# Optimization experiments

Measured on AMD Instinct MI355X. Metric: run time of the kernel, lower is better.

Reference implementation:

```python
import jax, jax.numpy as jnp
import numpy as np

N = 50000      # nodes
E = 800000     # edges (avg degree 16)
D = 128        # embed_dim
H = 8          # nhead
HD = D // H    # head dim = 16


def setup_inputs() -> dict:
    key = jax.random.key(0)
    ks = jax.random.split(key, 6)
    s = 1.0 / np.sqrt(D)  # ~xavier scale for square matrices
    return {
        "feats": jax.random.normal(ks[0], (N, D), jnp.float32),
        "edge_index": jax.random.randint(ks[1], (E, 2), 0, N, dtype=jnp.int64),
        "Wq": jax.random.normal(ks[2], (D, D), jnp.float32) * s,
        "bq": jnp.zeros((D,), jnp.float32),
        "Wk": jax.random.normal(ks[3], (D, D), jnp.float32) * s,
        "bk": jnp.zeros((D,), jnp.float32),
        "Wv": jax.random.normal(ks[4], (D, D), jnp.float32) * s,
        "bv": jnp.zeros((D,), jnp.float32),
        "Wo": jax.random.normal(ks[5], (D, D), jnp.float32) * s,
        "bo": jnp.zeros((D,), jnp.float32),
    }


def reference(feats, edge_index, Wq, bq, Wk, bk, Wv, bv, Wo, bo):
    # Projections (nn.Linear: x @ W.T + b), split into heads: [N, H, HD]
    q = (feats @ Wq.T + bq).reshape(N, H, HD)
    k = (feats @ Wk.T + bk).reshape(N, H, HD)
    v = (feats @ Wv.T + bv).reshape(N, H, HD)

    r = edge_index[:, 0]  # source nodes
    c = edge_index[:, 1]  # destination nodes (softmax / aggregation groups)

    # Per-edge, per-head dot-product scores: [E, H]
    scores = jnp.einsum('ehd,ehd->eh', q[c], k[r]) / np.sqrt(HD)

    # Custom scatter-softmax: src_max clamped to min 0; extra exp(-src_max) in denom
    smax = jnp.maximum(jax.ops.segment_max(scores, c, num_segments=N), 0.0)  # [N, H]
    ex = jnp.exp(scores - smax[c])                                           # [E, H]
    denom = jax.ops.segment_sum(ex, c, num_segments=N)                       # [N, H]
    attn = ex / (denom + jnp.exp(-smax))[c]                                  # [E, H]

    # Weighted V per edge, scatter-mean to destination nodes
    out_e = attn[:, :, None] * v[r]                      # [E, H, HD]
    agg = jax.ops.segment_sum(out_e, c, num_segments=N)  # [N, H, HD]
    cnt = jax.ops.segment_sum(jnp.ones((E,), jnp.float32), c, num_segments=N)
    agg = agg / jnp.maximum(cnt, 1.0)[:, None, None]

    return agg.reshape(N, D) @ Wo.T + bo
```

## Files before the change

kernel.cpp:

```cpp
#include <hip/hip_runtime.h>
#include <hip/hip_bf16.h>

#define N_NODES 50000
#define N_EDGES 800000
#define DIM 128
#define NHEAD 8
#define HDIM 16
#define ELL_PAD 64
#define ELL_SLICES 391
#define ELL_BLOCKS (8 * ELL_SLICES)
#define ROWTILES 3125
#define QKV_TPB 8
#define QKV_GROUPS ((ROWTILES + QKV_TPB - 1) / QKV_TPB)
#define QKV_GRID (QKV_GROUPS * 3)
#define OUT_BLOCKS ((ROWTILES + 3) / 4)

#define Q_OFF      0ull
#define KV_OFF     12800000ull
#define AGG_OFF    38400000ull
#define ELL_OFF    51200000ull
#define CNT_OFF    64000000ull
#define WBF_OFF    64200192ull
#define BIAS_OFF   64331264ull


typedef __attribute__((ext_vector_type(8))) short short8;
typedef __attribute__((ext_vector_type(4))) float floatx4;

__device__ inline float bflo2f(unsigned u) { return __uint_as_float(u << 16); }
__device__ inline float bfhi2f(unsigned u) { return __uint_as_float(u & 0xffff0000u); }
__device__ inline unsigned short f2bf(float f) {
    unsigned u = __float_as_uint(f);
    return (unsigned short)((u + 0x7fffu + ((u >> 16) & 1u)) >> 16);
}

__device__ inline void detect_flags(const void* feats, const void* edge,
                                    int& isbf, int& is32) {
    const unsigned short* f = (const unsigned short*)feats;
    const unsigned int* eg = (const unsigned int*)edge;
    int lane = threadIdx.x & 63;
    unsigned e = (f[lane] >> 7) & 0xFF;
    int junk = (e >= 0x90 || (e > 0 && e <= 0x60)) ? 1 : 0;
    unsigned long long jm = __ballot(junk);
    int nz = (lane < 32 && eg[2 * lane + 1] != 0) ? 1 : 0;
    unsigned long long nm = __ballot(nz);
    isbf = (jm == 0ull) ? 1 : 0;
    is32 = (nm != 0ull) ? 1 : 0;
}

__device__ inline void load_edge(const int* edge, int is32, int e, int& r, int& c) {
    if (is32) { int2 p = ((const int2*)edge)[e]; r = p.x; c = p.y; }
    else {
        const long long* p = (const long long*)edge;
        r = (int)p[2 * e]; c = (int)p[2 * e + 1];
    }
    if ((unsigned)r >= N_NODES) r = 0;
    if ((unsigned)c >= N_NODES) c = 0;
}

__device__ inline float ldf(const void* p, int isbf, int i) {
    return isbf ? __bfloat162float(((const __hip_bfloat16*)p)[i])
                : ((const float*)p)[i];
}

__device__ inline short8 ldfrag(const void* base, int isbf, size_t off) {
    if (isbf) return *(const short8*)((const unsigned short*)base + off);
    const float* f = (const float*)base + off;
    float4 f0 = *(const float4*)f;
    float4 f1 = *(const float4*)(f + 4);
    short8 a;
    a[0] = (short)f2bf(f0.x); a[1] = (short)f2bf(f0.y);
    a[2] = (short)f2bf(f0.z); a[3] = (short)f2bf(f0.w);
    a[4] = (short)f2bf(f1.x); a[5] = (short)f2bf(f1.y);
    a[6] = (short)f2bf(f1.z); a[7] = (short)f2bf(f1.w);
    return a;
}

__global__ __launch_bounds__(256) void ell_build(const void* feats, const int* edge,
                                                 const void* wq, const void* wk,
                                                 const void* wv, const void* wo,
                                                 const void* bq, const void* bk,
                                                 const void* bv, const void* bo,
                                                 int* cnt, int* ell,
                                                 unsigned short* wbf, float* bias) {
    int isbf, is32; detect_flags(feats, edge, isbf, is32);

    if (blockIdx.x >= ELL_BLOCKS) {
        int b2 = blockIdx.x - ELL_BLOCKS;
        if (b2 == 256) {
            for (int j = threadIdx.x; j < 512; j += 256) {
                int m2 = j >> 7;
                const void* bb = (m2 == 0) ? bq : (m2 == 1) ? bk : (m2 == 2) ? bv : bo;
                bias[j] = ldf(bb, isbf, j & 127);
            }
            return;
        }
        if (isbf) return;
        int idx = b2 * 256 + (int)threadIdx.x;
        int mm = idx >> 14, rem = idx & 16383;
        const void* wsrc = (mm == 0) ? wq : (mm == 1) ? wk : (mm == 2) ? wv : wo;
        wbf[idx] = f2bf(((const float*)wsrc)[rem]);
        return;
    }

    int pid = blockIdx.x & 7, slice = blockIdx.x >> 3;
    int base = slice * 2048 + (int)threadIdx.x;
    #pragma unroll
    for (int j = 0; j < 8; ++j) {
        int e = base + j * 256;
        if (e < N_EDGES) {
            int r, c; load_edge(edge, is32, e, r, c);
            if ((c & 7) == pid) {
                int slot = atomicAdd(cnt + c, 1);
                if (slot < ELL_PAD) ell[c * ELL_PAD + slot] = r;
            }
        }
    }
}

__global__ __launch_bounds__(256) void qkv_mfma(const void* feats_raw, const int* edge,
                                                const void* wq_raw, const void* wk_raw,
                                                const void* wv_raw,
                                                const unsigned short* wbf,
                                                const float* bias,
                                                unsigned short* q_s, unsigned short* kv_s) {
    int isbf, is32; detect_flags(feats_raw, edge, isbf, is32);
    int grp = blockIdx.x % QKV_GROUPS;
    int m   = blockIdx.x / QKV_GROUPS;
    int wv  = threadIdx.x >> 6;
    int lane = threadIdx.x & 63;
    int mrow = lane & 15, quad = lane >> 4;

    int rt0 = grp * QKV_TPB + wv * 2;
    int rt1 = rt0 + 1;
    bool v0 = rt0 < ROWTILES, v1 = rt1 < ROWTILES;

    short8 a0[4], a1[4];
    {
        size_t ar0 = (size_t)(v0 ? rt0 : 0) * 16 + mrow;
        size_t ar1 = (size_t)(v1 ? rt1 : 0) * 16 + mrow;
        #pragma unroll
        for (int kt = 0; kt < 4; ++kt) {
            a0[kt] = ldfrag(feats_raw, isbf, ar0 * DIM + quad * 8 + kt * 32);
            a1[kt] = ldfrag(feats_raw, isbf, ar1 * DIM + quad * 8 + kt * 32);
        }
    }

    const void* wraw = (m == 0) ? wq_raw : (m == 1) ? wk_raw : wv_raw;
    const unsigned short* wm = isbf ? (const unsigned short*)wraw : wbf + m * 16384;
    int pbase = (m == 2) ? 2 : 0;
    int piece = pbase + (mrow >> 3);
    int d = mrow & 7;

    for (int nt = 0; nt < 8; ++nt) {
        float b = bias[m * 128 + nt * 16 + mrow];
        floatx4 ac0 = {b, b, b, b};
        floatx4 ac1 = {b, b, b, b};
        const unsigned short* wp = wm + (size_t)(nt * 16 + mrow) * DIM + quad * 8;
        #pragma unroll
        for (int kt = 0; kt < 4; ++kt) {
            short8 bf = *(const short8*)(wp + kt * 32);
            ac0 = __builtin_amdgcn_mfma_f32_16x16x32_bf16(a0[kt], bf, ac0, 0, 0, 0);
            ac1 = __builtin_amdgcn_mfma_f32_16x16x32_bf16(a1[kt], bf, ac1, 0, 0, 0);
        }
        if (m == 0) {
            if (v0) {
                #pragma unroll
                for (int r4 = 0; r4 < 4; ++r4)
                    q_s[(size_t)(rt0 * 16 + quad * 4 + r4) * DIM + nt * 16 + mrow] = f2bf(ac0[r4]);
            }
            if (v1) {
                #pragma unroll
                for (int r4 = 0; r4 < 4; ++r4)
                    q_s[(size_t)(rt1 * 16 + quad * 4 + r4) * DIM + nt * 16 + mrow] = f2bf(ac1[r4]);
            }
        } else {
            if (v0) {
                #pragma unroll
                for (int r4 = 0; r4 < 4; ++r4)
                    kv_s[(size_t)(rt0 * 16 + quad * 4 + r4) * 256 + piece * 64 + nt * 8 + d] = f2bf(ac0[r4]);
            }
            if (v1) {
                #pragma unroll
                for (int r4 = 0; r4 < 4; ++r4)
                    kv_s[(size_t)(rt1 * 16 + quad * 4 + r4) * 256 + piece * 64 + nt * 8 + d] = f2bf(ac1[r4]);
            }
        }
    }
}

__global__ __launch_bounds__(256) void node_agg(const int* __restrict__ cnt,
                                                const int* __restrict__ ell,
                                                const unsigned short* __restrict__ q_s,
                                                const uint4* __restrict__ kvpack,
                                                uint4* __restrict__ agg_bf) {
    int node = (blockIdx.x * 256 + threadIdx.x) >> 6;
    int lane = threadIdx.x & 63;
    if (node >= N_NODES) return;
    int e = lane >> 3, h = lane & 7;

    const uint4* qp = (const uint4*)(q_s + (size_t)node * DIM + h * HDIM);
    uint4 q0 = qp[0], q1 = qp[1];
    float qv[16];
    qv[0]  = bflo2f(q0.x); qv[1]  = bfhi2f(q0.x);
    qv[2]  = bflo2f(q0.y); qv[3]  = bfhi2f(q0.y);
    qv[4]  = bflo2f(q0.z); qv[5]  = bfhi2f(q0.z);
    qv[6]  = bflo2f(q0.w); qv[7]  = bfhi2f(q0.w);
    qv[8]  = bflo2f(q1.x); qv[9]  = bfhi2f(q1.x);
    qv[10] = bflo2f(q1.y); qv[11] = bfhi2f(q1.y);
    qv[12] = bflo2f(q1.z); qv[13] = bfhi2f(q1.z);
    qv[14] = bflo2f(q1.w); qv[15] = bfhi2f(q1.w);

    int degt = cnt[node];
    int deg = degt < ELL_PAD ? degt : ELL_PAD;
    float l = 0.f;
    float acc[16];
    #pragma unroll
    for (int i = 0; i < 16; ++i) acc[i] = 0.f;

    const int* erow = ell + node * ELL_PAD;
    for (int i0 = 0; i0 < deg; i0 += 16) {
        int i1 = i0 + e, i2 = i0 + 8 + e;
        bool ok1 = i1 < deg, ok2 = i2 < deg;
        int r1 = ok1 ? erow[i1] : 0;
        int r2 = ok2 ? erow[i2] : 0;
        const uint4* kp1 = kvpack + (size_t)r1 * 32;
        const uint4* kp2 = kvpack + (size_t)r2 * 32;
        uint4 ka1 = kp1[h], kb1 = kp1[8 + h], va1 = kp1[16 + h], vb1 = kp1[24 + h];
        uint4 ka2 = kp2[h], kb2 = kp2[8 + h], va2 = kp2[16 + h], vb2 = kp2[24 + h];

        float s1 = 0.f;
        s1 += bflo2f(ka1.x) * qv[0]  + bfhi2f(ka1.x) * qv[1];
        s1 += bflo2f(ka1.y) * qv[2]  + bfhi2f(ka1.y) * qv[3];
        s1 += bflo2f(ka1.z) * qv[4]  + bfhi2f(ka1.z) * qv[5];
        s1 += bflo2f(ka1.w) * qv[6]  + bfhi2f(ka1.w) * qv[7];
        s1 += bflo2f(kb1.x) * qv[8]  + bfhi2f(kb1.x) * qv[9];
        s1 += bflo2f(kb1.y) * qv[10] + bfhi2f(kb1.y) * qv[11];
        s1 += bflo2f(kb1.z) * qv[12] + bfhi2f(kb1.z) * qv[13];
        s1 += bflo2f(kb1.w) * qv[14] + bfhi2f(kb1.w) * qv[15];
        float p1 = ok1 ? __expf(s1 * 0.25f) : 0.f;
        l += p1;
        acc[0]  += p1 * bflo2f(va1.x); acc[1]  += p1 * bfhi2f(va1.x);
        acc[2]  += p1 * bflo2f(va1.y); acc[3]  += p1 * bfhi2f(va1.y);
        acc[4]  += p1 * bflo2f(va1.z); acc[5]  += p1 * bfhi2f(va1.z);
        acc[6]  += p1 * bflo2f(va1.w); acc[7]  += p1 * bfhi2f(va1.w);
        acc[8]  += p1 * bflo2f(vb1.x); acc[9]  += p1 * bfhi2f(vb1.x);
        acc[10] += p1 * bflo2f(vb1.y); acc[11] += p1 * bfhi2f(vb1.y);
        acc[12] += p1 * bflo2f(vb1.z); acc[13] += p1 * bfhi2f(vb1.z);
        acc[14] += p1 * bflo2f(vb1.w); acc[15] += p1 * bfhi2f(vb1.w);

        float s2 = 0.f;
        s2 += bflo2f(ka2.x) * qv[0]  + bfhi2f(ka2.x) * qv[1];
        s2 += bflo2f(ka2.y) * qv[2]  + bfhi2f(ka2.y) * qv[3];
        s2 += bflo2f(ka2.z) * qv[4]  + bfhi2f(ka2.z) * qv[5];
        s2 += bflo2f(ka2.w) * qv[6]  + bfhi2f(ka2.w) * qv[7];
        s2 += bflo2f(kb2.x) * qv[8]  + bfhi2f(kb2.x) * qv[9];
        s2 += bflo2f(kb2.y) * qv[10] + bfhi2f(kb2.y) * qv[11];
        s2 += bflo2f(kb2.z) * qv[12] + bfhi2f(kb2.z) * qv[13];
        s2 += bflo2f(kb2.w) * qv[14] + bfhi2f(kb2.w) * qv[15];
        float p2 = ok2 ? __expf(s2 * 0.25f) : 0.f;
        l += p2;
        acc[0]  += p2 * bflo2f(va2.x); acc[1]  += p2 * bfhi2f(va2.x);
        acc[2]  += p2 * bflo2f(va2.y); acc[3]  += p2 * bfhi2f(va2.y);
        acc[4]  += p2 * bflo2f(va2.z); acc[5]  += p2 * bfhi2f(va2.z);
        acc[6]  += p2 * bflo2f(va2.w); acc[7]  += p2 * bfhi2f(va2.w);
        acc[8]  += p2 * bflo2f(vb2.x); acc[9]  += p2 * bfhi2f(vb2.x);
        acc[10] += p2 * bflo2f(vb2.y); acc[11] += p2 * bfhi2f(vb2.y);
        acc[12] += p2 * bflo2f(vb2.z); acc[13] += p2 * bfhi2f(vb2.z);
        acc[14] += p2 * bflo2f(vb2.w); acc[15] += p2 * bfhi2f(vb2.w);
    }

    #pragma unroll
    for (int m = 8; m < 64; m <<= 1) {
        l += __shfl_xor(l, m);
        #pragma unroll
        for (int i = 0; i < 16; ++i) acc[i] += __shfl_xor(acc[i], m);
    }

    float inv = 1.0f / ((1.0f + l) * (float)(degt > 0 ? degt : 1));
    if (e == 0) {
        unsigned o[8];
        #pragma unroll
        for (int i = 0; i < 8; ++i)
            o[i] = (unsigned)f2bf(acc[2 * i] * inv) | ((unsigned)f2bf(acc[2 * i + 1] * inv) << 16);
        uint4* op = agg_bf + (size_t)node * 16 + h * 2;
        op[0] = make_uint4(o[0], o[1], o[2], o[3]);
        op[1] = make_uint4(o[4], o[5], o[6], o[7]);
    }
}

__global__ __launch_bounds__(256) void out_mfma(const unsigned short* agg_bf,
                                                const void* feats, const int* edge,
                                                const void* wo_raw,
                                                const unsigned short* wbf,
                                                const float* bias, void* out) {
    int isbf, is32; detect_flags(feats, edge, isbf, is32);
    const unsigned short* W = isbf ? (const unsigned short*)wo_raw : wbf + 3 * 16384;
    int rowtile = blockIdx.x * 4 + (threadIdx.x >> 6);
    int lane = threadIdx.x & 63;
    int mrow = lane & 15, quad = lane >> 4;
    bool valid = rowtile < ROWTILES;
    size_t arow = (size_t)(valid ? rowtile : 0) * 16 + mrow;

    short8 a[4];
    const unsigned short* ap = agg_bf + arow * DIM + quad * 8;
    #pragma unroll
    for (int kt = 0; kt < 4; ++kt) a[kt] = *(const short8*)(ap + kt * 32);

    for (int nt = 0; nt < 8; nt += 2) {
        float b0 = bias[3 * 128 + nt * 16 + mrow];
        float b1 = bias[3 * 128 + (nt + 1) * 16 + mrow];
        floatx4 ac0 = {b0, b0, b0, b0};
        floatx4 ac1 = {b1, b1, b1, b1};
        const unsigned short* wp0 = W + (size_t)(nt * 16 + mrow) * DIM + quad * 8;
        const unsigned short* wp1 = W + (size_t)((nt + 1) * 16 + mrow) * DIM + quad * 8;
        #pragma unroll
        for (int kt = 0; kt < 4; ++kt) {
            short8 f0 = *(const short8*)(wp0 + kt * 32);
            short8 f1 = *(const short8*)(wp1 + kt * 32);
            ac0 = __builtin_amdgcn_mfma_f32_16x16x32_bf16(a[kt], f0, ac0, 0, 0, 0);
            ac1 = __builtin_amdgcn_mfma_f32_16x16x32_bf16(a[kt], f1, ac1, 0, 0, 0);
        }
        if (valid) {
            if (isbf) {
                #pragma unroll
                for (int r4 = 0; r4 < 4; ++r4) {
                    int row = rowtile * 16 + quad * 4 + r4;
                    ((unsigned short*)out)[(size_t)row * DIM + nt * 16 + mrow] = f2bf(ac0[r4]);
                    ((unsigned short*)out)[(size_t)row * DIM + (nt + 1) * 16 + mrow] = f2bf(ac1[r4]);
                }
            } else {
                #pragma unroll
                for (int r4 = 0; r4 < 4; ++r4) {
                    int row = rowtile * 16 + quad * 4 + r4;
                    ((float*)out)[(size_t)row * DIM + nt * 16 + mrow] = ac0[r4];
                    ((float*)out)[(size_t)row * DIM + (nt + 1) * 16 + mrow] = ac1[r4];
                }
            }
        }
    }
}

extern "C" void kernel_launch(void* const* d_in, const int* in_sizes, int n_in,
                              void* d_out, int out_size, void* d_ws, size_t ws_size,
                              hipStream_t stream) {
    const void* feats = d_in[0];
    const int*  edge  = (const int*)d_in[1];
    const void* Wq = d_in[2]; const void* bq = d_in[3];
    const void* Wk = d_in[4]; const void* bk = d_in[5];
    const void* Wv = d_in[6]; const void* bv = d_in[7];
    const void* Wo = d_in[8]; const void* bo = d_in[9];

    char* ws = (char*)d_ws;
    unsigned short* q_s  = (unsigned short*)(ws + Q_OFF);
    unsigned short* kv_s = (unsigned short*)(ws + KV_OFF);
    unsigned short* aggb = (unsigned short*)(ws + AGG_OFF);
    int* ell             = (int*)(ws + ELL_OFF);
    int* cnt             = (int*)(ws + CNT_OFF);
    unsigned short* wbf  = (unsigned short*)(ws + WBF_OFF);
    float* bias          = (float*)(ws + BIAS_OFF);

    hipMemsetAsync(ws + CNT_OFF, 0, N_NODES * 4, stream);

    ell_build<<<ELL_BLOCKS + 257, 256, 0, stream>>>(feats, edge, Wq, Wk, Wv, Wo,
                                                    bq, bk, bv, bo, cnt, ell,
                                                    wbf, bias);

    qkv_mfma<<<QKV_GRID, 256, 0, stream>>>(feats, edge, Wq, Wk, Wv, wbf, bias,
                                           q_s, kv_s);

    node_agg<<<(N_NODES * 64 + 255) / 256, 256, 0, stream>>>(cnt, ell, q_s,
                                                             (const uint4*)(ws + KV_OFF),
                                                             (uint4*)aggb);

    out_mfma<<<OUT_BLOCKS, 256, 0, stream>>>(aggb, feats, edge, Wo, wbf, bias, d_out);
}
```

Measured before the change: 241.4 us.

## Merge ELL build and QKV projection into one launch; pack bf16 math into float2

The ELL construction, weight conversion and QKV MFMA projection now run as separate block ranges of one kernel, so they overlap and one launch boundary disappears. The QKV blocks therefore convert raw weights and biases themselves through ldfrag/ldf instead of reading the pre-converted wbf buffer. The node aggregation loop is rewritten with float2 vectors, so the compiler can emit packed FMA instructions for the dot products and V accumulation. The cost is redundant fp32-to-bf16 weight conversion in every QKV block, and a different summation order in the scores.

```diff
diff --git a/kernel.cpp b/kernel.cpp
--- a/kernel.cpp
+++ b/kernel.cpp
@@ -13,6 +13,8 @@
 #define QKV_TPB 8
 #define QKV_GROUPS ((ROWTILES + QKV_TPB - 1) / QKV_TPB)
 #define QKV_GRID (QKV_GROUPS * 3)
+#define WBF_BLOCKS 257
+#define PREP_GRID (ELL_BLOCKS + WBF_BLOCKS + QKV_GRID)
 #define OUT_BLOCKS ((ROWTILES + 3) / 4)
 
 #define Q_OFF      0ull
@@ -26,12 +28,19 @@
 
 typedef __attribute__((ext_vector_type(8))) short short8;
 typedef __attribute__((ext_vector_type(4))) float floatx4;
+typedef __attribute__((ext_vector_type(2))) float floatx2;
 
 __device__ inline float bflo2f(unsigned u) { return __uint_as_float(u << 16); }
 __device__ inline float bfhi2f(unsigned u) { return __uint_as_float(u & 0xffff0000u); }
 __device__ inline unsigned short f2bf(float f) {
     unsigned u = __float_as_uint(f);
     return (unsigned short)((u + 0x7fffu + ((u >> 16) & 1u)) >> 16);
+}
+__device__ inline floatx2 bfpair(unsigned u) {
+    floatx2 r;
+    r.x = __uint_as_float(u << 16);
+    r.y = __uint_as_float(u & 0xffff0000u);
+    return r;
 }
 
 __device__ inline void detect_flags(const void* feats, const void* edge,
@@ -76,17 +85,36 @@
     return a;
 }
 
-__global__ __launch_bounds__(256) void ell_build(const void* feats, const int* edge,
-                                                 const void* wq, const void* wk,
-                                                 const void* wv, const void* wo,
-                                                 const void* bq, const void* bk,
-                                                 const void* bv, const void* bo,
-                                                 int* cnt, int* ell,
-                                                 unsigned short* wbf, float* bias) {
-    int isbf, is32; detect_flags(feats, edge, isbf, is32);
-
-    if (blockIdx.x >= ELL_BLOCKS) {
-        int b2 = blockIdx.x - ELL_BLOCKS;
+__global__ __launch_bounds__(256) void prep(const void* feats_raw, const int* edge,
+                                            const void* wq_raw, const void* wk_raw,
+                                            const void* wv_raw, const void* wo_raw,
+                                            const void* bq, const void* bk,
+                                            const void* bv, const void* bo,
+                                            int* cnt, int* ell,
+                                            unsigned short* wbf, float* bias,
+                                            unsigned short* q_s, unsigned short* kv_s) {
+    int isbf, is32; detect_flags(feats_raw, edge, isbf, is32);
+    int blk = blockIdx.x;
+
+    if (blk < ELL_BLOCKS) {
+        int pid = blk & 7, slice = blk >> 3;
+        int base = slice * 2048 + (int)threadIdx.x;
+        #pragma unroll
+        for (int j = 0; j < 8; ++j) {
+            int e = base + j * 256;
+            if (e < N_EDGES) {
+                int r, c; load_edge(edge, is32, e, r, c);
+                if ((c & 7) == pid) {
+                    int slot = atomicAdd(cnt + c, 1);
+                    if (slot < ELL_PAD) ell[c * ELL_PAD + slot] = r;
+                }
+            }
+        }
+        return;
+    }
+
+    if (blk < ELL_BLOCKS + WBF_BLOCKS) {
+        int b2 = blk - ELL_BLOCKS;
         if (b2 == 256) {
             for (int j = threadIdx.x; j < 512; j += 256) {
                 int m2 = j >> 7;
@@ -98,35 +126,14 @@
         if (isbf) return;
         int idx = b2 * 256 + (int)threadIdx.x;
         int mm = idx >> 14, rem = idx & 16383;
-        const void* wsrc = (mm == 0) ? wq : (mm == 1) ? wk : (mm == 2) ? wv : wo;
+        const void* wsrc = (mm == 0) ? wq_raw : (mm == 1) ? wk_raw : (mm == 2) ? wv_raw : wo_raw;
         wbf[idx] = f2bf(((const float*)wsrc)[rem]);
         return;
     }
 
-    int pid = blockIdx.x & 7, slice = blockIdx.x >> 3;
-    int base = slice * 2048 + (int)threadIdx.x;
-    #pragma unroll
-    for (int j = 0; j < 8; ++j) {
-        int e = base + j * 256;
-        if (e < N_EDGES) {
-            int r, c; load_edge(edge, is32, e, r, c);
-            if ((c & 7) == pid) {
-                int slot = atomicAdd(cnt + c, 1);
-                if (slot < ELL_PAD) ell[c * ELL_PAD + slot] = r;
-            }
-        }
-    }
-}
-
-__global__ __launch_bounds__(256) void qkv_mfma(const void* feats_raw, const int* edge,
-                                                const void* wq_raw, const void* wk_raw,
-                                                const void* wv_raw,
-                                                const unsigned short* wbf,
-                                                const float* bias,
-                                                unsigned short* q_s, unsigned short* kv_s) {
-    int isbf, is32; detect_flags(feats_raw, edge, isbf, is32);
-    int grp = blockIdx.x % QKV_GROUPS;
-    int m   = blockIdx.x / QKV_GROUPS;
+    int qb = blk - ELL_BLOCKS - WBF_BLOCKS;
+    int grp = qb % QKV_GROUPS;
+    int m   = qb / QKV_GROUPS;
     int wv  = threadIdx.x >> 6;
     int lane = threadIdx.x & 63;
     int mrow = lane & 15, quad = lane >> 4;
@@ -147,19 +154,19 @@
     }
 
     const void* wraw = (m == 0) ? wq_raw : (m == 1) ? wk_raw : wv_raw;
-    const unsigned short* wm = isbf ? (const unsigned short*)wraw : wbf + m * 16384;
+    const void* braw = (m == 0) ? bq : (m == 1) ? bk : bv;
     int pbase = (m == 2) ? 2 : 0;
     int piece = pbase + (mrow >> 3);
     int d = mrow & 7;
 
     for (int nt = 0; nt < 8; ++nt) {
-        float b = bias[m * 128 + nt * 16 + mrow];
+        float b = ldf(braw, isbf, nt * 16 + mrow);
         floatx4 ac0 = {b, b, b, b};
         floatx4 ac1 = {b, b, b, b};
-        const unsigned short* wp = wm + (size_t)(nt * 16 + mrow) * DIM + quad * 8;
         #pragma unroll
         for (int kt = 0; kt < 4; ++kt) {
-            short8 bf = *(const short8*)(wp + kt * 32);
+            short8 bf = ldfrag(wraw, isbf,
+                               (size_t)(nt * 16 + mrow) * DIM + quad * 8 + kt * 32);
             ac0 = __builtin_amdgcn_mfma_f32_16x16x32_bf16(a0[kt], bf, ac0, 0, 0, 0);
             ac1 = __builtin_amdgcn_mfma_f32_16x16x32_bf16(a1[kt], bf, ac1, 0, 0, 0);
         }
@@ -201,22 +208,18 @@
 
     const uint4* qp = (const uint4*)(q_s + (size_t)node * DIM + h * HDIM);
     uint4 q0 = qp[0], q1 = qp[1];
-    float qv[16];
-    qv[0]  = bflo2f(q0.x); qv[1]  = bfhi2f(q0.x);
-    qv[2]  = bflo2f(q0.y); qv[3]  = bfhi2f(q0.y);
-    qv[4]  = bflo2f(q0.z); qv[5]  = bfhi2f(q0.z);
-    qv[6]  = bflo2f(q0.w); qv[7]  = bfhi2f(q0.w);
-    qv[8]  = bflo2f(q1.x); qv[9]  = bfhi2f(q1.x);
-    qv[10] = bflo2f(q1.y); qv[11] = bfhi2f(q1.y);
-    qv[12] = bflo2f(q1.z); qv[13] = bfhi2f(q1.z);
-    qv[14] = bflo2f(q1.w); qv[15] = bfhi2f(q1.w);
+    floatx2 qv[8];
+    qv[0] = bfpair(q0.x); qv[1] = bfpair(q0.y);
+    qv[2] = bfpair(q0.z); qv[3] = bfpair(q0.w);
+    qv[4] = bfpair(q1.x); qv[5] = bfpair(q1.y);
+    qv[6] = bfpair(q1.z); qv[7] = bfpair(q1.w);
 
     int degt = cnt[node];
     int deg = degt < ELL_PAD ? degt : ELL_PAD;
     float l = 0.f;
-    float acc[16];
+    floatx2 acc[8];
     #pragma unroll
-    for (int i = 0; i < 16; ++i) acc[i] = 0.f;
+    for (int i = 0; i < 8; ++i) acc[i] = (floatx2){0.f, 0.f};
 
     const int* erow = ell + node * ELL_PAD;
     for (int i0 = 0; i0 < deg; i0 += 16) {
@@ -229,52 +232,49 @@
         uint4 ka1 = kp1[h], kb1 = kp1[8 + h], va1 = kp1[16 + h], vb1 = kp1[24 + h];
         uint4 ka2 = kp2[h], kb2 = kp2[8 + h], va2 = kp2[16 + h], vb2 = kp2[24 + h];
 
-        float s1 = 0.f;
-        s1 += bflo2f(ka1.x) * qv[0]  + bfhi2f(ka1.x) * qv[1];
-        s1 += bflo2f(ka1.y) * qv[2]  + bfhi2f(ka1.y) * qv[3];
-        s1 += bflo2f(ka1.z) * qv[4]  + bfhi2f(ka1.z) * qv[5];
-        s1 += bflo2f(ka1.w) * qv[6]  + bfhi2f(ka1.w) * qv[7];
-        s1 += bflo2f(kb1.x) * qv[8]  + bfhi2f(kb1.x) * qv[9];
-        s1 += bflo2f(kb1.y) * qv[10] + bfhi2f(kb1.y) * qv[11];
-        s1 += bflo2f(kb1.z) * qv[12] + bfhi2f(kb1.z) * qv[13];
-        s1 += bflo2f(kb1.w) * qv[14] + bfhi2f(kb1.w) * qv[15];
+        floatx2 d1 = bfpair(ka1.x) * qv[0];
+        d1 += bfpair(ka1.y) * qv[1];
+        d1 += bfpair(ka1.z) * qv[2];
+        d1 += bfpair(ka1.w) * qv[3];
+        d1 += bfpair(kb1.x) * qv[4];
+        d1 += bfpair(kb1.y) * qv[5];
+        d1 += bfpair(kb1.z) * qv[6];
+        d1 += bfpair(kb1.w) * qv[7];
+        float s1 = d1.x + d1.y;
         float p1 = ok1 ? __expf(s1 * 0.25f) : 0.f;
         l += p1;
-        acc[0]  += p1 * bflo2f(va1.x); acc[1]  += p1 * bfhi2f(va1.x);
-        acc[2]  += p1 * bflo2f(va1.y); acc[3]  += p1 * bfhi2f(va1.y);
-        acc[4]  += p1 * bflo2f(va1.z); acc[5]  += p1 * bfhi2f(va1.z);
-        acc[6]  += p1 * bflo2f(va1.w); acc[7]  += p1 * bfhi2f(va1.w);
-        acc[8]  += p1 * bflo2f(vb1.x); acc[9]  += p1 * bfhi2f(vb1.x);
-        acc[10] += p1 * bflo2f(vb1.y); acc[11] += p1 * bfhi2f(vb1.y);
-        acc[12] += p1 * bflo2f(vb1.z); acc[13] += p1 * bfhi2f(vb1.z);
-        acc[14] += p1 * bflo2f(vb1.w); acc[15] += p1 * bfhi2f(vb1.w);
-
-        float s2 = 0.f;
-        s2 += bflo2f(ka2.x) * qv[0]  + bfhi2f(ka2.x) * qv[1];
-        s2 += bflo2f(ka2.y) * qv[2]  + bfhi2f(ka2.y) * qv[3];
-        s2 += bflo2f(ka2.z) * qv[4]  + bfhi2f(ka2.z) * qv[5];
-        s2 += bflo2f(ka2.w) * qv[6]  + bfhi2f(ka2.w) * qv[7];
-        s2 += bflo2f(kb2.x) * qv[8]  + bfhi2f(kb2.x) * qv[9];
-        s2 += bflo2f(kb2.y) * qv[10] + bfhi2f(kb2.y) * qv[11];
-        s2 += bflo2f(kb2.z) * qv[12] + bfhi2f(kb2.z) * qv[13];
-        s2 += bflo2f(kb2.w) * qv[14] + bfhi2f(kb2.w) * qv[15];
+        floatx2 p1v = {p1, p1};
+        acc[0] += p1v * bfpair(va1.x); acc[1] += p1v * bfpair(va1.y);
+        acc[2] += p1v * bfpair(va1.z); acc[3] += p1v * bfpair(va1.w);
+        acc[4] += p1v * bfpair(vb1.x); acc[5] += p1v * bfpair(vb1.y);
+        acc[6] += p1v * bfpair(vb1.z); acc[7] += p1v * bfpair(vb1.w);
+
+        floatx2 d2 = bfpair(ka2.x) * qv[0];
+        d2 += bfpair(ka2.y) * qv[1];
+        d2 += bfpair(ka2.z) * qv[2];
+        d2 += bfpair(ka2.w) * qv[3];
+        d2 += bfpair(kb2.x) * qv[4];
+        d2 += bfpair(kb2.y) * qv[5];
+        d2 += bfpair(kb2.z) * qv[6];
+        d2 += bfpair(kb2.w) * qv[7];
+        float s2 = d2.x + d2.y;
         float p2 = ok2 ? __expf(s2 * 0.25f) : 0.f;
         l += p2;
-        acc[0]  += p2 * bflo2f(va2.x); acc[1]  += p2 * bfhi2f(va2.x);
-        acc[2]  += p2 * bflo2f(va2.y); acc[3]  += p2 * bfhi2f(va2.y);
-        acc[4]  += p2 * bflo2f(va2.z); acc[5]  += p2 * bfhi2f(va2.z);
-        acc[6]  += p2 * bflo2f(va2.w); acc[7]  += p2 * bfhi2f(va2.w);
-        acc[8]  += p2 * bflo2f(vb2.x); acc[9]  += p2 * bfhi2f(vb2.x);
-        acc[10] += p2 * bflo2f(vb2.y); acc[11] += p2 * bfhi2f(vb2.y);
-        acc[12] += p2 * bflo2f(vb2.z); acc[13] += p2 * bfhi2f(vb2.z);
-        acc[14] += p2 * bflo2f(vb2.w); acc[15] += p2 * bfhi2f(vb2.w);
+        floatx2 p2v = {p2, p2};
+        acc[0] += p2v * bfpair(va2.x); acc[1] += p2v * bfpair(va2.y);
+        acc[2] += p2v * bfpair(va2.z); acc[3] += p2v * bfpair(va2.w);
+        acc[4] += p2v * bfpair(vb2.x); acc[5] += p2v * bfpair(vb2.y);
+        acc[6] += p2v * bfpair(vb2.z); acc[7] += p2v * bfpair(vb2.w);
     }
 
     #pragma unroll
     for (int m = 8; m < 64; m <<= 1) {
         l += __shfl_xor(l, m);
         #pragma unroll
-        for (int i = 0; i < 16; ++i) acc[i] += __shfl_xor(acc[i], m);
+        for (int i = 0; i < 8; ++i) {
+            acc[i].x += __shfl_xor(acc[i].x, m);
+            acc[i].y += __shfl_xor(acc[i].y, m);
+        }
     }
 
     float inv = 1.0f / ((1.0f + l) * (float)(degt > 0 ? degt : 1));
@@ -282,7 +282,7 @@
         unsigned o[8];
         #pragma unroll
         for (int i = 0; i < 8; ++i)
-            o[i] = (unsigned)f2bf(acc[2 * i] * inv) | ((unsigned)f2bf(acc[2 * i + 1] * inv) << 16);
+            o[i] = (unsigned)f2bf(acc[i].x * inv) | ((unsigned)f2bf(acc[i].y * inv) << 16);
         uint4* op = agg_bf + (size_t)node * 16 + h * 2;
         op[0] = make_uint4(o[0], o[1], o[2], o[3]);
         op[1] = make_uint4(o[4], o[5], o[6], o[7]);
@@ -362,12 +362,9 @@
 
     hipMemsetAsync(ws + CNT_OFF, 0, N_NODES * 4, stream);
 
-    ell_build<<<ELL_BLOCKS + 257, 256, 0, stream>>>(feats, edge, Wq, Wk, Wv, Wo,
-                                                    bq, bk, bv, bo, cnt, ell,
-                                                    wbf, bias);
-
-    qkv_mfma<<<QKV_GRID, 256, 0, stream>>>(feats, edge, Wq, Wk, Wv, wbf, bias,
-                                           q_s, kv_s);
+    prep<<<PREP_GRID, 256, 0, stream>>>(feats, edge, Wq, Wk, Wv, Wo,
+                                        bq, bk, bv, bo, cnt, ell, wbf, bias,
+                                        q_s, kv_s);
 
     node_agg<<<(N_NODES * 64 + 255) / 256, 256, 0, stream>>>(cnt, ell, q_s,
                                                              (const uint4*)(ws + KV_OFF),
```

Result: slower. 265.1 us (+9.8%).
